# Performance work log

Hardware: AMD Instinct MI355X
Metric: run time of the kernel (lower is better)

Reference implementation:

```python
import jax, jax.numpy as jnp
import numpy as np

K = 32
EPS = 1e-5  # BatchNorm eps; eval mode with running_mean=0, running_var=1


def knn_idx(x):
    # x: [B, C, N] -> idx of K nearest neighbors [B, N, K]
    inner = -2.0 * jnp.einsum('bcn,bcm->bnm', x, x)
    xx = jnp.sum(x * x, axis=1)  # [B, N]
    pd = -xx[:, :, None] - inner - xx[:, None, :]  # negative squared dist
    return jax.lax.top_k(pd, K)[1]


def get_neighbors(x):
    # x: [B, C, N] -> edge features [B, N, K, 2C] (nbr - ctr, ctr)
    idx = knn_idx(x)
    xt = jnp.transpose(x, (0, 2, 1))  # [B, N, C]
    nbrs = jax.vmap(lambda p, i: p[i])(xt, idx)  # [B, N, K, C]
    ctr = jnp.broadcast_to(xt[:, :, None, :], nbrs.shape)
    return jnp.concatenate([nbrs - ctr, ctr], axis=-1)


def bn_eval(h, g, b, nd):
    # inference-mode BN, running_mean=0, running_var=1
    shape = [1, -1] + [1] * (nd - 2)
    return h * (g / jnp.sqrt(1.0 + EPS)).reshape(shape) + b.reshape(shape)


def edge_conv(x, W, g, b):
    # x: [B, C, N] -> [B, O, N]; 1x1 conv over edge feats + BN + LeakyReLU + max over K
    feat = get_neighbors(x)  # [B, N, K, 2C]
    h = jnp.einsum('bnkc,oc->bonk', feat, W)
    h = jax.nn.leaky_relu(bn_eval(h, g, b, 4), 0.2)
    return jnp.max(h, axis=-1)


def setup_inputs():
    key = jax.random.key(0)
    ks = jax.random.split(key, 40)
    B, N = 4, 2048

    def rn(i, shape, s=0.1):
        return jax.random.normal(ks[i], shape, jnp.float32) * s

    def gm(i, c):
        return 1.0 + rn(i, (c,))

    inp = {
        'x': jax.random.normal(ks[0], (B, 3, N), jnp.float32),
        'l': jax.random.normal(ks[1], (B, 5), jnp.float32),
        'n': jax.random.normal(ks[2], (B, 7), jnp.float32),
        'W1': rn(3, (64, 6)), 'g1': gm(4, 64), 'b1': rn(5, (64,)),
        'W2': rn(6, (64, 128)), 'g2': gm(7, 64), 'b2': rn(8, (64,)),
        'W3': rn(9, (128, 128)), 'g3': gm(10, 128), 'b3': rn(11, (128,)),
        'W4': rn(12, (256, 256)), 'g4': gm(13, 256), 'b4': rn(14, (256,)),
        'W5': rn(15, (1024, 512)), 'g5': gm(16, 1024), 'b5': rn(17, (1024,)),
        'W6': rn(18, (64, 5)), 'g6': gm(19, 64), 'b6': rn(20, (64,)),
        'W7': rn(21, (64, 7)), 'g7': gm(22, 64), 'b7': rn(23, (64,)),
        'L1': rn(24, (512, 1152)), 'g8': gm(25, 512), 'b8': rn(26, (512,)),
        'L2': rn(27, (256, 512)), 'L2b': rn(28, (256,)), 'g9': gm(29, 256), 'b9': rn(30, (256,)),
        'L3': rn(31, (28, 256)), 'L3b': rn(32, (28,)),
    }
    return inp


def reference(x, l, n, W1, g1, b1, W2, g2, b2, W3, g3, b3, W4, g4, b4,
              W5, g5, b5, W6, g6, b6, W7, g7, b7,
              L1, g8, b8, L2, L2b, g9, b9, L3, L3b):
    x1 = edge_conv(x, W1, g1, b1)    # [B, 64, N]
    x2 = edge_conv(x1, W2, g2, b2)   # [B, 64, N]
    x3 = edge_conv(x2, W3, g3, b3)   # [B, 128, N]
    x4 = edge_conv(x3, W4, g4, b4)   # [B, 256, N]
    cat = jnp.concatenate([x1, x2, x3, x4], axis=1)  # [B, 512, N]
    h = jnp.einsum('bcn,oc->bon', cat, W5)
    h = jax.nn.leaky_relu(bn_eval(h, g5, b5, 3), 0.2)
    h = jnp.max(h, axis=-1)  # global max pool -> [B, 1024]
    lf = jax.nn.leaky_relu(bn_eval(jnp.einsum('bc,oc->bo', l, W6), g6, b6, 2), 0.2)
    nf = jax.nn.leaky_relu(bn_eval(jnp.einsum('bc,oc->bo', n, W7), g7, b7, 2), 0.2)
    v = jnp.concatenate([h, lf, nf], axis=-1)  # [B, 1152]
    v = jax.nn.relu(bn_eval(v @ L1.T, g8, b8, 2))  # dropout = identity (eval)
    v = jax.nn.relu(bn_eval(v @ L2.T + L2b, g9, b9, 2))
    return v @ L3.T + L3b  # [B, 28]
```

## Files before the change

kernel.cpp:

```cpp
#include <hip/hip_runtime.h>
#include <hip/hip_bf16.h>

#define NPTS 2048
#define NB 4
#define KNN 32
#define NIN 33

static __device__ __forceinline__ float b2f(__hip_bfloat16 v) { return __bfloat162float(v); }
#define ISQ 0.99999499996875f

typedef __attribute__((ext_vector_type(8))) short short8v;
typedef __attribute__((ext_vector_type(4))) float f32x4;

static __device__ __forceinline__ unsigned ordkey(float f) {
  unsigned u = __float_as_uint(f);
  return u ^ (unsigned)(((int)u >> 31) | 0x80000000);
}

static __device__ __forceinline__ void loadv(const float* p, float (&d)[1]) { d[0] = *p; }
static __device__ __forceinline__ void loadv(const float* p, float (&d)[2]) {
  float2 v = *(const float2*)p; d[0] = v.x; d[1] = v.y;
}
static __device__ __forceinline__ void loadv(const float* p, float (&d)[4]) {
  float4 v = *(const float4*)p; d[0] = v.x; d[1] = v.y; d[2] = v.z; d[3] = v.w;
}

static __device__ __forceinline__ float wave_red_sum(float s) {
#pragma unroll
  for (int off = 32; off > 0; off >>= 1) s += __shfl_xor(s, off);
  return s;
}

__global__ __launch_bounds__(64) void detect_kernel(const unsigned short* __restrict__ x,
                                                    int* __restrict__ flag) {
  int cnt = 0;
  for (int i = threadIdx.x; i < 512; i += 64) {
    unsigned e = (x[i] >> 7) & 0xFFu;
    if (e >= 0xC6u) cnt++;
  }
#pragma unroll
  for (int off = 32; off > 0; off >>= 1) cnt += __shfl_down(cnt, off);
  if (threadIdx.x == 0) flag[0] = (cnt == 0) ? 1 : 0;
}

struct CvtArgs {
  const void* src[NIN];
  int off[NIN + 1];
};

__global__ __launch_bounds__(256) void cvt_all_kernel(CvtArgs a, float* __restrict__ out,
                                                      int total, int nb1,
                                                      __hip_bfloat16* __restrict__ w5bf,
                                                      const int* __restrict__ flag) {
  if ((int)blockIdx.x < nb1) {
    int t = blockIdx.x * 256 + threadIdx.x;
    if (t >= total) return;
    int s = 0;
    while (t >= a.off[s + 1]) s++;
    int j = t - a.off[s];
    float v;
    if (flag[0]) v = b2f(((const __hip_bfloat16*)a.src[s])[j]);
    else         v = ((const float*)a.src[s])[j];
    out[t] = v;
  } else {
    int t = (blockIdx.x - nb1) * 256 + threadIdx.x;
    if (flag[0]) w5bf[t] = ((const __hip_bfloat16*)a.src[15])[t];
    else         w5bf[t] = __float2bfloat16(((const float*)a.src[15])[t]);
  }
}

template <int C>
__global__ __launch_bounds__(256) void xx_kernel(const float* __restrict__ x, long bstride,
                                                 float* __restrict__ xx) {
  int t = blockIdx.x * 256 + threadIdx.x;
  int b = t / NPTS, m = t % NPTS;
  const float* xb = x + (long)b * bstride + m;
  float s = 0.f;
#pragma unroll
  for (int c = 0; c < C; ++c) { float v = xb[(long)c * NPTS]; s = fmaf(v, v, s); }
  xx[t] = s;
}

template <int C>
__global__ __launch_bounds__(256) void pdgemmsym_kernel(const float* __restrict__ x, long bstride,
                                                        const float* __restrict__ xx,
                                                        unsigned* __restrict__ keys) {
  constexpr int KT = (C < 16) ? C : 16;
  __shared__ __align__(16) float At[KT][64];
  __shared__ __align__(16) float Bt[KT][64];
  __shared__ __align__(16) unsigned Ts[64][68];
  int t = blockIdx.x;
  int tj = (int)((sqrtf(8.f * (float)t + 1.f) - 1.f) * 0.5f);
  while ((tj + 1) * (tj + 2) / 2 <= t) tj++;
  while (tj * (tj + 1) / 2 > t) tj--;
  int ti = t - tj * (tj + 1) / 2;
  int n0 = ti * 64, m0 = tj * 64;
  int tid = threadIdx.x, tx = tid & 15, ty = tid >> 4;
  const float* xb = x + (long)blockIdx.y * bstride;
  float acc[4][4] = {};
  for (int k0 = 0; k0 < C; k0 += KT) {
    for (int lin = tid; lin < KT * 64; lin += 256) {
      int r = lin >> 6, col = lin & 63;
      At[r][col] = xb[(long)(k0 + r) * NPTS + n0 + col];
      Bt[r][col] = xb[(long)(k0 + r) * NPTS + m0 + col];
    }
    __syncthreads();
#pragma unroll
    for (int kc = 0; kc < KT; ++kc) {
      float4 av = *(const float4*)&At[kc][ty * 4];
      float4 bv = *(const float4*)&Bt[kc][tx * 4];
      acc[0][0] = fmaf(av.x, bv.x, acc[0][0]); acc[0][1] = fmaf(av.x, bv.y, acc[0][1]);
      acc[0][2] = fmaf(av.x, bv.z, acc[0][2]); acc[0][3] = fmaf(av.x, bv.w, acc[0][3]);
      acc[1][0] = fmaf(av.y, bv.x, acc[1][0]); acc[1][1] = fmaf(av.y, bv.y, acc[1][1]);
      acc[1][2] = fmaf(av.y, bv.z, acc[1][2]); acc[1][3] = fmaf(av.y, bv.w, acc[1][3]);
      acc[2][0] = fmaf(av.z, bv.x, acc[2][0]); acc[2][1] = fmaf(av.z, bv.y, acc[2][1]);
      acc[2][2] = fmaf(av.z, bv.z, acc[2][2]); acc[2][3] = fmaf(av.z, bv.w, acc[2][3]);
      acc[3][0] = fmaf(av.w, bv.x, acc[3][0]); acc[3][1] = fmaf(av.w, bv.y, acc[3][1]);
      acc[3][2] = fmaf(av.w, bv.z, acc[3][2]); acc[3][3] = fmaf(av.w, bv.w, acc[3][3]);
    }
    __syncthreads();
  }
  const float* xxq = xx + (long)blockIdx.y * NPTS;
  float4 xxm = *(const float4*)&xxq[m0 + tx * 4];
  unsigned* kb = keys + ((long)blockIdx.y << 22);
  unsigned ok[4][4];
#pragma unroll
  for (int i = 0; i < 4; ++i) {
    float xxn = xxq[n0 + ty * 4 + i];
    ok[i][0] = ordkey((-xxn - (-2.f * acc[i][0])) - xxm.x);
    ok[i][1] = ordkey((-xxn - (-2.f * acc[i][1])) - xxm.y);
    ok[i][2] = ordkey((-xxn - (-2.f * acc[i][2])) - xxm.z);
    ok[i][3] = ordkey((-xxn - (-2.f * acc[i][3])) - xxm.w);
    uint4 o = make_uint4(ok[i][0], ok[i][1], ok[i][2], ok[i][3]);
    *(uint4*)&kb[(long)(n0 + ty * 4 + i) * NPTS + m0 + tx * 4] = o;
  }
  if (ti != tj) {
#pragma unroll
    for (int i = 0; i < 4; ++i)
#pragma unroll
      for (int j = 0; j < 4; ++j) Ts[tx * 4 + j][ty * 4 + i] = ok[i][j];
    __syncthreads();
#pragma unroll
    for (int i = 0; i < 4; ++i)
      *(uint4*)&kb[(long)(m0 + ty * 4 + i) * NPTS + n0 + tx * 4] =
          *(const uint4*)&Ts[ty * 4 + i][tx * 4];
  }
}

__global__ __launch_bounds__(256) void select_kernel(const unsigned* __restrict__ keys,
                                                     int* __restrict__ idxout) {
  int wave = threadIdx.x >> 6, lane = threadIdx.x & 63;
  int q = blockIdx.x * 4 + wave;
  int bloc = q >> 11, n = q & 2047;
  const uint4* rp = (const uint4*)(keys + ((long)((bloc << 11) | n) << 11));
  unsigned K[32];
#pragma unroll
  for (int t = 0; t < 8; ++t) {
    uint4 kk = rp[t * 64 + lane];
    K[4 * t + 0] = kk.x; K[4 * t + 1] = kk.y; K[4 * t + 2] = kk.z; K[4 * t + 3] = kk.w;
  }
  unsigned t0 = 0, t1 = 0, t2 = 0, t3 = 0;
#pragma unroll
  for (int s = 0; s < 32; ++s) {
    unsigned k = K[s];
    if (k > t3) {
      if (k > t1) {
        if (k > t0) { t3 = t2; t2 = t1; t1 = t0; t0 = k; }
        else        { t3 = t2; t2 = t1; t1 = k; }
      } else {
        if (k > t2) { t3 = t2; t2 = k; }
        else        { t3 = k; }
      }
    }
  }
  unsigned orv = t0 | t1 | t2 | t3, andv = t0 & t1 & t2 & t3;
#pragma unroll
  for (int xm = 32; xm >= 1; xm >>= 1) {
    orv  |= __shfl_xor(orv, xm);
    andv &= __shfl_xor(andv, xm);
  }
  unsigned V = orv ^ andv;
  unsigned P = andv & ~V;
  int need = KNN;
  for (int b = 31; b >= 0; --b) {
    unsigned bit = 1u << b;
    if (!(V & bit)) continue;
    unsigned hm = 0xFFFFFFFFu << b;
    unsigned Pb = (P & hm) | bit;
    int c = (int)__popcll(__ballot((t0 & hm) == Pb)) +
            (int)__popcll(__ballot((t1 & hm) == Pb)) +
            (int)__popcll(__ballot((t2 & hm) == Pb)) +
            (int)__popcll(__ballot((t3 & hm) == Pb));
    if (c >= need) P |= bit;
    else need -= c;
  }
  int cg = 0;
#pragma unroll
  for (int s = 0; s < 32; ++s) cg += (int)__popcll(__ballot(K[s] > P));
  if (cg > KNN - 1) {
    unsigned orf = K[0], anf = K[0];
#pragma unroll
    for (int s = 1; s < 32; ++s) { orf |= K[s]; anf &= K[s]; }
#pragma unroll
    for (int xm = 32; xm >= 1; xm >>= 1) {
      orf |= __shfl_xor(orf, xm);
      anf &= __shfl_xor(anf, xm);
    }
    unsigned Vf = orf ^ anf;
    P = anf & ~Vf;
    need = KNN;
    for (int b = 31; b >= 0; --b) {
      unsigned bit = 1u << b;
      if (!(Vf & bit)) continue;
      unsigned hm = 0xFFFFFFFFu << b;
      unsigned Pb = (P & hm) | bit;
      int c = 0;
#pragma unroll
      for (int s = 0; s < 32; ++s) c += (int)__popcll(__ballot((K[s] & hm) == Pb));
      if (c >= need) P |= bit;
      else need -= c;
    }
  }
  int* orow = idxout + ((bloc << 11) | n) * KNN;
  int base = 0;
  unsigned eqmask = 0;
#pragma unroll
  for (int s = 0; s < 32; ++s) {
    bool take = K[s] > P;
    unsigned long long bal = __ballot(take);
    if (take) {
      int pos = base + (int)__popcll(bal & ((1ull << lane) - 1ull));
      orow[pos] = ((s >> 2) << 8) + lane * 4 + (s & 3);
    }
    base += (int)__popcll(bal);
    if (K[s] == P) eqmask |= (1u << s);
  }
  int rem = KNN - base;
  for (int it = 0; it < rem; ++it) {
    unsigned mym = 0xFFFFFFFFu;
    if (eqmask) {
      int s = __ffs(eqmask) - 1;
      mym = (unsigned)(((s >> 2) << 8) + lane * 4 + (s & 3));
    }
    unsigned wm = mym;
#pragma unroll
    for (int xm = 32; xm >= 1; xm >>= 1) {
      unsigned o = __shfl_xor(wm, xm);
      wm = o < wm ? o : wm;
    }
    if (mym == wm) {
      orow[base + it] = (int)wm;
      eqmask &= eqmask - 1;
    }
  }
}

template <int C>
__global__ __launch_bounds__(256) void yzt_kernel(const float* __restrict__ x, long bstride,
                                                  const float* __restrict__ W, int O,
                                                  float* __restrict__ yt, float* __restrict__ zt) {
  constexpr int KT = (C < 16) ? C : 16;
  __shared__ __align__(16) float Xs[KT][64];
  __shared__ __align__(16) float Wy[KT][64];
  __shared__ __align__(16) float Wp[KT][64];
  int b = blockIdx.z, m0 = blockIdx.y * 64, o0 = blockIdx.x * 64;
  int tid = threadIdx.x, tx = tid & 15, ty = tid >> 4;
  const float* xb = x + (long)b * bstride;
  const int twoC = 2 * C;
  float accy[4][4] = {}, accp[4][4] = {};
  for (int k0 = 0; k0 < C; k0 += KT) {
    for (int lin = tid; lin < KT * 64; lin += 256) {
      int r = lin >> 6, col = lin & 63;
      Xs[r][col] = xb[(long)(k0 + r) * NPTS + m0 + col];
      float wy = W[(o0 + col) * twoC + k0 + r];
      Wy[r][col] = wy;
      Wp[r][col] = W[(o0 + col) * twoC + C + k0 + r] - wy;
    }
    __syncthreads();
#pragma unroll
    for (int kc = 0; kc < KT; ++kc) {
      float4 wv = *(const float4*)&Wy[kc][tx * 4];
      float4 pv = *(const float4*)&Wp[kc][tx * 4];
      float xm[4];
      xm[0] = Xs[kc][ty * 4 + 0]; xm[1] = Xs[kc][ty * 4 + 1];
      xm[2] = Xs[kc][ty * 4 + 2]; xm[3] = Xs[kc][ty * 4 + 3];
#pragma unroll
      for (int i = 0; i < 4; ++i) {
        accy[i][0] = fmaf(xm[i], wv.x, accy[i][0]);
        accy[i][1] = fmaf(xm[i], wv.y, accy[i][1]);
        accy[i][2] = fmaf(xm[i], wv.z, accy[i][2]);
        accy[i][3] = fmaf(xm[i], wv.w, accy[i][3]);
        accp[i][0] = fmaf(xm[i], pv.x, accp[i][0]);
        accp[i][1] = fmaf(xm[i], pv.y, accp[i][1]);
        accp[i][2] = fmaf(xm[i], pv.z, accp[i][2]);
        accp[i][3] = fmaf(xm[i], pv.w, accp[i][3]);
      }
    }
    __syncthreads();
  }
#pragma unroll
  for (int i = 0; i < 4; ++i) {
    long base = ((long)b * NPTS + m0 + ty * 4 + i) * O + o0 + tx * 4;
    *(float4*)&yt[base] = make_float4(accy[i][0], accy[i][1], accy[i][2], accy[i][3]);
    *(float4*)&zt[base] = make_float4(accp[i][0], accp[i][1], accp[i][2], accp[i][3]);
  }
}

template <int RO>
__global__ __launch_bounds__(256) void gmaxt_kernel(const float* __restrict__ yt,
                                                    const float* __restrict__ zt,
                                                    const int* __restrict__ idx,
                                                    const float* __restrict__ g,
                                                    const float* __restrict__ bb,
                                                    float* __restrict__ out, long obstride,
                                                    float* __restrict__ xxout,
                                                    __hip_bfloat16* __restrict__ catbf, int loff) {
  constexpr int O = RO * 64;
  int wave = threadIdx.x >> 6, lane = threadIdx.x & 63;
  int n = blockIdx.x * 4 + wave, b = blockIdx.y;
  int jreg = idx[((b << 11) + n) * KNN + (lane & 31)];
  int obase = lane * RO;
  float gs[RO], bs[RO], zr[RO], acc[RO];
  loadv(zt + ((long)(b << 11) + n) * O + obase, zr);
#pragma unroll
  for (int r = 0; r < RO; ++r) {
    gs[r] = g[obase + r] * ISQ;
    bs[r] = bb[obase + r];
    acc[r] = -INFINITY;
  }
  const float* yb = yt + ((long)(b << 11)) * O + obase;
#pragma unroll
  for (int k = 0; k < KNN; ++k) {
    int j = __shfl(jreg, k);
    float yv[RO];
    loadv(yb + (long)j * O, yv);
#pragma unroll
    for (int r = 0; r < RO; ++r) {
      float v = fmaf(gs[r], yv[r] + zr[r], bs[r]);
      v = v >= 0.f ? v : 0.2f * v;
      acc[r] = fmaxf(acc[r], v);
    }
  }
  float* op = out + (long)b * obstride + (long)obase * NPTS + n;
#pragma unroll
  for (int r = 0; r < RO; ++r) op[(long)r * NPTS] = acc[r];
  __hip_bfloat16* cb = catbf + ((long)(b << 11) + n) * 512 + loff + obase;
#pragma unroll
  for (int r = 0; r < RO; ++r) cb[r] = __float2bfloat16(acc[r]);
  if (xxout) {
    float ss = 0.f;
#pragma unroll
    for (int r = 0; r < RO; ++r) ss = fmaf(acc[r], acc[r], ss);
    ss = wave_red_sum(ss);
    if (lane == 0) xxout[(b << 11) + n] = ss;
  }
}

__global__ __launch_bounds__(256) void gemm5m_kernel(const __hip_bfloat16* __restrict__ catbf,
                                                     const __hip_bfloat16* __restrict__ w5bf,
                                                     const float* __restrict__ g5,
                                                     const float* __restrict__ b5,
                                                     float* __restrict__ pmax) {
  int b = blockIdx.z, po0 = blockIdx.y * 128, n0 = blockIdx.x * 64;
  int wave = threadIdx.x >> 6, lane = threadIdx.x & 63;
  int quad = lane >> 4, l15 = lane & 15;
  const short* wp0 = (const short*)w5bf + (long)(po0 + wave * 32 + l15) * 512 + quad * 8;
  const short* wp1 = wp0 + 16 * 512;
  const short* cp = (const short*)catbf + ((long)(b << 11) + n0 + l15) * 512 + quad * 8;
  f32x4 acc[2][4] = {};
  short8v ca0 = *(const short8v*)wp0;
  short8v ca1 = *(const short8v*)wp1;
  short8v cb[4];
#pragma unroll
  for (int nt = 0; nt < 4; ++nt) cb[nt] = *(const short8v*)(cp + nt * 16 * 512);
  for (int k0 = 0; k0 < 512; k0 += 32) {
    int kn = (k0 + 32 < 512) ? k0 + 32 : 0;
    short8v na0 = *(const short8v*)(wp0 + kn);
    short8v na1 = *(const short8v*)(wp1 + kn);
    short8v nb[4];
#pragma unroll
    for (int nt = 0; nt < 4; ++nt) nb[nt] = *(const short8v*)(cp + nt * 16 * 512 + kn);
#pragma unroll
    for (int nt = 0; nt < 4; ++nt) {
      acc[0][nt] = __builtin_amdgcn_mfma_f32_16x16x32_bf16(ca0, cb[nt], acc[0][nt], 0, 0, 0);
      acc[1][nt] = __builtin_amdgcn_mfma_f32_16x16x32_bf16(ca1, cb[nt], acc[1][nt], 0, 0, 0);
    }
    ca0 = na0; ca1 = na1;
#pragma unroll
    for (int nt = 0; nt < 4; ++nt) cb[nt] = nb[nt];
  }
#pragma unroll
  for (int i = 0; i < 2; ++i) {
#pragma unroll
    for (int r = 0; r < 4; ++r) {
      int po = po0 + wave * 32 + i * 16 + quad * 4 + r;
      float sc = g5[po] * ISQ;
      float bi = b5[po];
      float mx = -INFINITY;
#pragma unroll
      for (int nt = 0; nt < 4; ++nt) {
        float v = fmaf(sc, acc[i][nt][r], bi);
        v = v >= 0.f ? v : 0.2f * v;
        mx = fmaxf(mx, v);
      }
#pragma unroll
      for (int xm = 1; xm < 16; xm <<= 1) mx = fmaxf(mx, __shfl_xor(mx, xm));
      if (l15 == 0) pmax[(long)(b * 1024 + po) * 32 + blockIdx.x] = mx;
    }
  }
}

__global__ __launch_bounds__(256) void redlfnf_kernel(const float* __restrict__ pmax,
                                                      const float* __restrict__ l,
                                                      const float* __restrict__ nn,
                                                      const float* __restrict__ W6,
                                                      const float* __restrict__ g6,
                                                      const float* __restrict__ b6,
                                                      const float* __restrict__ W7,
                                                      const float* __restrict__ g7,
                                                      const float* __restrict__ b7,
                                                      float* __restrict__ v) {
  if (blockIdx.x < 16) {
    int t = blockIdx.x * 256 + threadIdx.x;
    float mx = -INFINITY;
#pragma unroll
    for (int j = 0; j < 32; ++j) mx = fmaxf(mx, pmax[(long)t * 32 + j]);
    int b = t >> 10, po = t & 1023;
    v[b * 1152 + po] = mx;
  } else {
    int idx = (blockIdx.x - 16) * 256 + threadIdx.x;
    int b = idx >> 7, t = idx & 127;
    if (t < 64) {
      float s = 0.f;
#pragma unroll
      for (int c = 0; c < 5; ++c) s = fmaf(W6[t * 5 + c], l[b * 5 + c], s);
      float val = fmaf(g6[t] * ISQ, s, b6[t]);
      v[b * 1152 + 1024 + t] = val >= 0.f ? val : 0.2f * val;
    } else {
      int o = t - 64;
      float s = 0.f;
#pragma unroll
      for (int c = 0; c < 7; ++c) s = fmaf(W7[o * 7 + c], nn[b * 7 + c], s);
      float val = fmaf(g7[o] * ISQ, s, b7[o]);
      v[b * 1152 + 1088 + o] = val >= 0.f ? val : 0.2f * val;
    }
  }
}

__global__ __launch_bounds__(256) void head1_kernel(const float* __restrict__ v,
                                                    const float* __restrict__ L1,
                                                    const float* __restrict__ g8,
                                                    const float* __restrict__ b8,
                                                    float* __restrict__ v1) {
  int wave = threadIdx.x >> 6, lane = threadIdx.x & 63;
  int t = blockIdx.x * 4 + wave;
  int b = t >> 9, o = t & 511;
  const float* vb = v + b * 1152;
  const float* wr = L1 + (long)o * 1152;
  float s = 0.f;
#pragma unroll
  for (int c = lane; c < 1152; c += 64) s = fmaf(wr[c], vb[c], s);
  s = wave_red_sum(s);
  if (lane == 0) {
    float val = fmaf(g8[o] * ISQ, s, b8[o]);
    v1[t] = fmaxf(val, 0.f);
  }
}

__global__ __launch_bounds__(256) void head2_kernel(const float* __restrict__ v1,
                                                    const float* __restrict__ L2,
                                                    const float* __restrict__ L2b,
                                                    const float* __restrict__ g9,
                                                    const float* __restrict__ b9,
                                                    float* __restrict__ v2) {
  int wave = threadIdx.x >> 6, lane = threadIdx.x & 63;
  int t = blockIdx.x * 4 + wave;
  int b = t >> 8, o = t & 255;
  const float* vb = v1 + b * 512;
  const float* wr = L2 + (long)o * 512;
  float s = 0.f;
#pragma unroll
  for (int c = lane; c < 512; c += 64) s = fmaf(wr[c], vb[c], s);
  s = wave_red_sum(s);
  if (lane == 0) {
    float sv = s + L2b[o];
    float val = fmaf(g9[o] * ISQ, sv, b9[o]);
    v2[t] = fmaxf(val, 0.f);
  }
}

__global__ __launch_bounds__(256) void head3_kernel(const float* __restrict__ v2,
                                                    const float* __restrict__ L3,
                                                    const float* __restrict__ L3b,
                                                    void* __restrict__ out,
                                                    const int* __restrict__ flag) {
  int wave = threadIdx.x >> 6, lane = threadIdx.x & 63;
  int t = blockIdx.x * 4 + wave;
  if (t >= 112) return;
  int b = t / 28, o = t % 28;
  const float* vb = v2 + b * 256;
  const float* wr = L3 + o * 256;
  float s = 0.f;
#pragma unroll
  for (int c = lane; c < 256; c += 64) s = fmaf(wr[c], vb[c], s);
  s = wave_red_sum(s);
  if (lane == 0) {
    float sv = s + L3b[o];
    if (flag[0]) ((__hip_bfloat16*)out)[t] = __float2bfloat16(sv);
    else         ((float*)out)[t] = sv;
  }
}

extern "C" void kernel_launch(void* const* d_in, const int* in_sizes, int n_in,
                              void* d_out, int out_size, void* d_ws, size_t ws_size,
                              hipStream_t stream) {
  CvtArgs ca;
  int off[NIN + 1];
  off[0] = 0;
  for (int i = 0; i < NIN; ++i) {
    ca.src[i] = d_in[i];
    off[i + 1] = off[i] + in_sizes[i];
    ca.off[i] = off[i];
  }
  ca.off[NIN] = off[NIN];
  const int total = off[NIN];

  int* flag = (int*)d_ws;
  float* fin = (float*)((char*)d_ws + 64);
  const float* xf  = fin + off[0];
  const float* lf  = fin + off[1];
  const float* nf  = fin + off[2];
  const float* W1f = fin + off[3];  const float* g1f = fin + off[4];  const float* b1f = fin + off[5];
  const float* W2f = fin + off[6];  const float* g2f = fin + off[7];  const float* b2f_ = fin + off[8];
  const float* W3f = fin + off[9];  const float* g3f = fin + off[10]; const float* b3f = fin + off[11];
  const float* W4f = fin + off[12]; const float* g4f = fin + off[13]; const float* b4f = fin + off[14];
  const float* g5f = fin + off[16]; const float* b5f = fin + off[17];
  const float* W6f = fin + off[18]; const float* g6f = fin + off[19]; const float* b6f = fin + off[20];
  const float* W7f = fin + off[21]; const float* g7f = fin + off[22]; const float* b7f = fin + off[23];
  const float* L1f = fin + off[24]; const float* g8f = fin + off[25]; const float* b8f = fin + off[26];
  const float* L2f = fin + off[27]; const float* L2bf = fin + off[28];
  const float* g9f = fin + off[29]; const float* b9f = fin + off[30];
  const float* L3f = fin + off[31]; const float* L3bf = fin + off[32];

  float* p = fin + ((total + 15) & ~15);
  float* cat  = p;
  float* yb   = cat + 4 * 512 * NPTS;
  float* zb   = yb + 4 * 256 * NPTS;
  float* xxb  = zb + 4 * 256 * NPTS;
  int*   idxb = (int*)(xxb + 4 * NPTS);
  float* pmax = (float*)(idxb + 4 * NPTS * KNN);
  float* vb   = pmax + 4 * 1024 * 32;
  float* v1b  = vb + 4 * 1152;
  float* v2b  = v1b + 4 * 512;
  __hip_bfloat16* w5bf  = (__hip_bfloat16*)(v2b + 4 * 256);
  __hip_bfloat16* catbf = w5bf + 1024 * 512;
  unsigned* keys_tail = (unsigned*)(catbf + (size_t)4 * NPTS * 512);

  size_t need_full = (size_t)((char*)(keys_tail + (size_t)NB * NPTS * NPTS) - (char*)d_ws);
  int bpass = (ws_size >= need_full) ? NB : 1;
  unsigned* keys = (bpass == NB) ? keys_tail : (unsigned*)yb;

  const long bst1 = 3L * NPTS;
  const long bstc = 512L * NPTS;
  const int NTRI = 32 * 33 / 2;
  const int nb1 = (total + 255) / 256;

  detect_kernel<<<1, 64, 0, stream>>>((const unsigned short*)d_in[0], flag);
  cvt_all_kernel<<<nb1 + 2048, 256, 0, stream>>>(ca, fin, total, nb1, w5bf, flag);

  xx_kernel<3><<<32, 256, 0, stream>>>(xf, bst1, xxb);
  for (int b0 = 0; b0 < NB; b0 += bpass) {
    pdgemmsym_kernel<3><<<dim3(NTRI, bpass), 256, 0, stream>>>(xf + b0 * bst1, bst1, xxb + b0 * NPTS, keys);
    select_kernel<<<512 * bpass, 256, 0, stream>>>(keys, idxb + (long)b0 * NPTS * KNN);
  }
  yzt_kernel<3><<<dim3(1, 32, NB), 256, 0, stream>>>(xf, bst1, W1f, 64, yb, zb);
  gmaxt_kernel<1><<<dim3(512, NB), 256, 0, stream>>>(yb, zb, idxb, g1f, b1f, cat, bstc, xxb, catbf, 0);

  for (int b0 = 0; b0 < NB; b0 += bpass) {
    pdgemmsym_kernel<64><<<dim3(NTRI, bpass), 256, 0, stream>>>(cat + b0 * bstc, bstc, xxb + b0 * NPTS, keys);
    select_kernel<<<512 * bpass, 256, 0, stream>>>(keys, idxb + (long)b0 * NPTS * KNN);
  }
  yzt_kernel<64><<<dim3(1, 32, NB), 256, 0, stream>>>(cat, bstc, W2f, 64, yb, zb);
  gmaxt_kernel<1><<<dim3(512, NB), 256, 0, stream>>>(yb, zb, idxb, g2f, b2f_, cat + 64L * NPTS, bstc, xxb, catbf, 64);

  for (int b0 = 0; b0 < NB; b0 += bpass) {
    pdgemmsym_kernel<64><<<dim3(NTRI, bpass), 256, 0, stream>>>(cat + 64L * NPTS + b0 * bstc, bstc, xxb + b0 * NPTS, keys);
    select_kernel<<<512 * bpass, 256, 0, stream>>>(keys, idxb + (long)b0 * NPTS * KNN);
  }
  yzt_kernel<64><<<dim3(2, 32, NB), 256, 0, stream>>>(cat + 64L * NPTS, bstc, W3f, 128, yb, zb);
  gmaxt_kernel<2><<<dim3(512, NB), 256, 0, stream>>>(yb, zb, idxb, g3f, b3f, cat + 128L * NPTS, bstc, xxb, catbf, 128);

  for (int b0 = 0; b0 < NB; b0 += bpass) {
    pdgemmsym_kernel<128><<<dim3(NTRI, bpass), 256, 0, stream>>>(cat + 128L * NPTS + b0 * bstc, bstc, xxb + b0 * NPTS, keys);
    select_kernel<<<512 * bpass, 256, 0, stream>>>(keys, idxb + (long)b0 * NPTS * KNN);
  }
  yzt_kernel<128><<<dim3(4, 32, NB), 256, 0, stream>>>(cat + 128L * NPTS, bstc, W4f, 256, yb, zb);
  gmaxt_kernel<4><<<dim3(512, NB), 256, 0, stream>>>(yb, zb, idxb, g4f, b4f, cat + 256L * NPTS, bstc, (float*)nullptr, catbf, 256);

  gemm5m_kernel<<<dim3(32, 8, NB), 256, 0, stream>>>(catbf, w5bf, g5f, b5f, pmax);
  redlfnf_kernel<<<18, 256, 0, stream>>>(pmax, lf, nf, W6f, g6f, b6f, W7f, g7f, b7f, vb);

  head1_kernel<<<512, 256, 0, stream>>>(vb, L1f, g8f, b8f, v1b);
  head2_kernel<<<256, 256, 0, stream>>>(v1b, L2f, L2bf, g9f, b9f, v2b);
  head3_kernel<<<28, 256, 0, stream>>>(v2b, L3f, L3bf, d_out, flag);
}
```

Measured before the change: 559.2 us.

## Stage shared B tile in LDS with double buffering in gemm5m kernel

The conv5 GEMM kernel now loads the catbf tile for the block's 64 points once per block into a double-buffered shared-memory buffer, instead of each of the four waves loading the same B fragments from global memory on its own. K is processed in 64-wide steps, prefetching the next step's register data while MFMAs run on the current LDS buffer, with one block barrier per step. This cuts redundant global or L2 traffic for the activation operand, at the cost of LDS reads, barriers and extra register pressure from prefetched A and B fragments.

```diff
diff --git a/kernel.cpp b/kernel.cpp
--- a/kernel.cpp
+++ b/kernel.cpp
@@ -361,45 +361,81 @@
                                                      const float* __restrict__ g5,
                                                      const float* __restrict__ b5,
                                                      float* __restrict__ pmax) {
+  __shared__ __align__(16) short Bs[2][8 * 64 * 8];
   int b = blockIdx.z, po0 = blockIdx.y * 128, n0 = blockIdx.x * 64;
   int wave = threadIdx.x >> 6, lane = threadIdx.x & 63;
   int quad = lane >> 4, l15 = lane & 15;
-  const short* wp0 = (const short*)w5bf + (long)(po0 + wave * 32 + l15) * 512 + quad * 8;
-  const short* wp1 = wp0 + 16 * 512;
-  const short* cp = (const short*)catbf + ((long)(b << 11) + n0 + l15) * 512 + quad * 8;
+  const short* cbase = (const short*)catbf + ((long)(b << 11) + n0) * 512;
+  const short* abase0 = (const short*)w5bf + (long)(po0 + wave * 32 + l15) * 512 + quad * 8;
+  const short* abase1 = abase0 + 16 * 512;
+  const short* bsrc0 = cbase + (long)lane * 512 + (2 * wave + 0) * 8;
+  const short* bsrc1 = cbase + (long)lane * 512 + (2 * wave + 1) * 8;
+  short* bdst0 = &Bs[0][((2 * wave + 0) * 64 + lane) * 8];
+  short* bdst1 = &Bs[0][((2 * wave + 1) * 64 + lane) * 8];
+  const int bufstride = 8 * 64 * 8;
+
+  short8v Br[2][2], Ar[2][2][2];
   f32x4 acc[2][4] = {};
-  short8v ca0 = *(const short8v*)wp0;
-  short8v ca1 = *(const short8v*)wp1;
-  short8v cb[4];
-#pragma unroll
-  for (int nt = 0; nt < 4; ++nt) cb[nt] = *(const short8v*)(cp + nt * 16 * 512);
-  for (int k0 = 0; k0 < 512; k0 += 32) {
-    int kn = (k0 + 32 < 512) ? k0 + 32 : 0;
-    short8v na0 = *(const short8v*)(wp0 + kn);
-    short8v na1 = *(const short8v*)(wp1 + kn);
-    short8v nb[4];
-#pragma unroll
-    for (int nt = 0; nt < 4; ++nt) nb[nt] = *(const short8v*)(cp + nt * 16 * 512 + kn);
-#pragma unroll
-    for (int nt = 0; nt < 4; ++nt) {
-      acc[0][nt] = __builtin_amdgcn_mfma_f32_16x16x32_bf16(ca0, cb[nt], acc[0][nt], 0, 0, 0);
-      acc[1][nt] = __builtin_amdgcn_mfma_f32_16x16x32_bf16(ca1, cb[nt], acc[1][nt], 0, 0, 0);
-    }
-    ca0 = na0; ca1 = na1;
-#pragma unroll
-    for (int nt = 0; nt < 4; ++nt) cb[nt] = nb[nt];
-  }
-#pragma unroll
-  for (int i = 0; i < 2; ++i) {
+
+  Br[0][0] = *(const short8v*)(bsrc0);
+  Br[0][1] = *(const short8v*)(bsrc1);
+#pragma unroll
+  for (int h = 0; h < 2; ++h)
+#pragma unroll
+    for (int j = 0; j < 2; ++j)
+      Ar[0][h][j] = *(const short8v*)((h ? abase1 : abase0) + j * 32);
+  *(short8v*)bdst0 = Br[0][0];
+  *(short8v*)bdst1 = Br[0][1];
+  Br[1][0] = *(const short8v*)(bsrc0 + 64);
+  Br[1][1] = *(const short8v*)(bsrc1 + 64);
+#pragma unroll
+  for (int h = 0; h < 2; ++h)
+#pragma unroll
+    for (int j = 0; j < 2; ++j)
+      Ar[1][h][j] = *(const short8v*)((h ? abase1 : abase0) + 64 + j * 32);
+  __syncthreads();
+
+  for (int it = 0; it < 8; ++it) {
+    int cur = it & 1;
+    const short* lb = &Bs[cur][0];
+#pragma unroll
+    for (int j = 0; j < 2; ++j) {
+#pragma unroll
+      for (int nt = 0; nt < 4; ++nt) {
+        short8v bf = *(const short8v*)(lb + ((j * 4 + quad) * 64 + nt * 16 + l15) * 8);
+        acc[0][nt] = __builtin_amdgcn_mfma_f32_16x16x32_bf16(Ar[cur][0][j], bf, acc[0][nt], 0, 0, 0);
+        acc[1][nt] = __builtin_amdgcn_mfma_f32_16x16x32_bf16(Ar[cur][1][j], bf, acc[1][nt], 0, 0, 0);
+      }
+    }
+    if (it < 7) {
+      if (it < 6) {
+        int ks = (it + 2) * 64;
+        Br[cur][0] = *(const short8v*)(bsrc0 + ks);
+        Br[cur][1] = *(const short8v*)(bsrc1 + ks);
+#pragma unroll
+        for (int h = 0; h < 2; ++h)
+#pragma unroll
+          for (int j = 0; j < 2; ++j)
+            Ar[cur][h][j] = *(const short8v*)((h ? abase1 : abase0) + ks + j * 32);
+      }
+      int nb = cur ^ 1;
+      *(short8v*)(bdst0 + nb * bufstride) = Br[nb][0];
+      *(short8v*)(bdst1 + nb * bufstride) = Br[nb][1];
+      __syncthreads();
+    }
+  }
+
+#pragma unroll
+  for (int h = 0; h < 2; ++h) {
 #pragma unroll
     for (int r = 0; r < 4; ++r) {
-      int po = po0 + wave * 32 + i * 16 + quad * 4 + r;
+      int po = po0 + wave * 32 + h * 16 + quad * 4 + r;
       float sc = g5[po] * ISQ;
       float bi = b5[po];
       float mx = -INFINITY;
 #pragma unroll
       for (int nt = 0; nt < 4; ++nt) {
-        float v = fmaf(sc, acc[i][nt][r], bi);
+        float v = fmaf(sc, acc[h][nt][r], bi);
         v = v >= 0.f ? v : 0.2f * v;
         mx = fmaxf(mx, v);
       }
```

After: 539.3 us. -3.6%, faster.
